# Performance work log

Measured on AMD Instinct MI355X. Metric: run time of the kernel, lower is better.

## Reference

```python
import jax, jax.numpy as jnp
import numpy as np

N = 16000      # nodes
E = 256000     # edges (avg degree 16)
C = 64         # channel multiplicity (64x0e node feats)
A = 10         # num elements (one-hot node_attrs)
R = 8          # num radial edge feats
OFFS = [0, 1, 4, 9]   # m-offsets for l=0,1,2 blocks (dims 1,3,5)
AVG_NEIGH = 16.0


def setup_inputs() -> dict:
    key = jax.random.key(0)
    ks = jax.random.split(key, 12)
    species = jax.random.randint(ks[0], (N,), 0, A)
    node_attrs = jax.nn.one_hot(species, A, dtype=jnp.float32)
    node_feats = jax.random.normal(ks[1], (N, C), jnp.float32)
    edge_attrs_real = jax.random.normal(ks[2], (E, 9), jnp.float32)
    edge_attrs_imag = jax.random.normal(ks[3], (E, 9), jnp.float32)
    edge_feats = jax.random.normal(ks[4], (E, R), jnp.float32)
    senders = jax.random.randint(ks[5], (E,), 0, N)
    receivers = jax.random.randint(ks[6], (E,), 0, N)
    # learned parameters
    W_up = jax.random.normal(ks[7], (C, C), jnp.float32)            # linear_up (64x0e -> 64x0e)
    W_tpw = jax.random.normal(ks[8], (A, R, 3, C), jnp.float32) * 0.1  # TensorProductWeightsBlock, weight_numel = 3*C
    W_lin = jax.random.normal(ks[9], (3, C, C), jnp.float32)        # per-l linear on irreps_mid -> irreps_out
    W_skip = jax.random.normal(ks[10], (C, A, C), jnp.float32)      # FullyConnectedTensorProduct skip
    return {"node_attrs": node_attrs, "node_feats": node_feats,
            "edge_attrs_real": edge_attrs_real, "edge_attrs_imag": edge_attrs_imag,
            "edge_feats": edge_feats, "senders": senders, "receivers": receivers,
            "W_up": W_up, "W_tpw": W_tpw, "W_lin": W_lin, "W_skip": W_skip}


def reference(node_attrs, node_feats, edge_attrs_real, edge_attrs_imag, edge_feats,
              senders, receivers, W_up, W_tpw, W_lin, W_skip):
    # skip connection: FullyConnectedTensorProduct(node_feats, node_attrs) (all scalars)
    sc = jnp.einsum('nu,na,uak->nk', node_feats, node_attrs, W_skip) / np.float32(np.sqrt(C * A))
    # linear_up (e3nn Linear with 1/sqrt(fan_in) normalization)
    h = (node_feats @ W_up) / np.float32(np.sqrt(C))
    # per-edge TP weights: einsum('be,ba,aek->bk'), reshaped to [E, 3 paths, C]
    tp_w = jnp.einsum('er,ea,arlu->elu', edge_feats, node_attrs[senders], W_tpw)
    x_s = h[senders]  # gather sender node feats [E, C]
    def conv(edge_attrs):
        # uvu tensor product 64x0e x (0e+1o+2e): CG(0,l,l)=1 -> weighted outer product per l
        parts = [x_s[:, :, None] * tp_w[:, l, :, None] * edge_attrs[:, None, OFFS[l]:OFFS[l + 1]]
                 for l in range(3)]
        mji = jnp.concatenate(parts, axis=-1)                      # [E, C, 9]
        m = jax.ops.segment_sum(mji, receivers, num_segments=N)   # scatter-sum -> [N, C, 9]
        outs = [jnp.einsum('num,uv->nvm', m[:, :, OFFS[l]:OFFS[l + 1]], W_lin[l]) / np.float32(np.sqrt(C))
                for l in range(3)]
        return jnp.concatenate(outs, axis=-1) / np.float32(AVG_NEIGH)  # [N, C, 9]
    message_real = conv(edge_attrs_real)
    message_imag = conv(edge_attrs_imag)
    # torch.view_as_complex + reshape_irreps -> complex [N, C, 9]; returned as (real, imag)
    return message_real, message_imag, sc
```

## Files before the change

### kernel.cpp

```cpp
#include <hip/hip_runtime.h>
#include <hip/hip_bf16.h>

#define NN 16000
#define EE 256000
#define CC 64
#define AA 10
#define RR 8
#define NC9 9216000
#define SC_OFF 18432000

#define WS_H        0
#define WS_BLK      4096000
#define WS_WLT      32768000
#define WS_SPECIES  32817152
#define WS_COUNTS   32881152
#define WS_CURSOR   32945152
#define WS_OFFSETS  33009152
#define WS_ELIST    33073216

__device__ __forceinline__ float comp4(float4 v, int j) {
  return j == 0 ? v.x : j == 1 ? v.y : j == 2 ? v.z : v.w;
}

__global__ __launch_bounds__(256) void prep_kernel(
    const float* __restrict__ attrs, const int* __restrict__ recv,
    const float* __restrict__ W_lin, int* __restrict__ species,
    int* __restrict__ counts, float* __restrict__ wlt) {
  int i = blockIdx.x * 256 + threadIdx.x;
  if (i < NN) {
    const float* p = attrs + (size_t)i * AA;
    int sp = 0;
#pragma unroll
    for (int a = 1; a < AA; ++a)
      if (p[a] > 0.5f) sp = a;
    species[i] = sp;
  }
  if (i < 3 * 64 * 64) {
    int l = i >> 12, rem = i & 4095, v = rem >> 6, u = rem & 63;
    wlt[i] = W_lin[l * 4096 + u * 64 + v];
  }
  if (i < EE) atomicAdd(&counts[recv[i]], 1);
}

__global__ __launch_bounds__(1024) void scan_kernel(
    const int* __restrict__ counts, int* __restrict__ offsets) {
  __shared__ int part[1024];
  int tid = threadIdx.x;
  const int CH = 16;
  int base = tid * CH;
  int loc[CH];
  int s = 0;
#pragma unroll
  for (int i = 0; i < CH; ++i) {
    int idx = base + i;
    int c = (idx < NN) ? counts[idx] : 0;
    loc[i] = c;
    s += c;
  }
  part[tid] = s;
  __syncthreads();
  for (int off = 1; off < 1024; off <<= 1) {
    int t = part[tid];
    int add = (tid >= off) ? part[tid - off] : 0;
    __syncthreads();
    part[tid] = t + add;
    __syncthreads();
  }
  int pre = (tid > 0) ? part[tid - 1] : 0;
#pragma unroll
  for (int i = 0; i < CH; ++i) {
    int idx = base + i;
    if (idx <= NN) offsets[idx] = pre;
    pre += loc[i];
  }
}

__global__ __launch_bounds__(256) void edge_kernel(
    const int* __restrict__ recv, const int* __restrict__ senders,
    const int* __restrict__ species, const int* __restrict__ offsets,
    int* __restrict__ cursor, int* __restrict__ elist,
    const float* __restrict__ ef, const float* __restrict__ ear,
    const float* __restrict__ eai, float* __restrict__ blk) {
  int e = blockIdx.x * 256 + threadIdx.x;
  if (e >= EE) return;
  int r = recv[e];
  int pos = atomicAdd(&cursor[r], 1);
  elist[offsets[r] + pos] = e;
  int s = senders[e];
  int a = species[s];
  const float* efp = ef + (size_t)e * 8;
  const float* erp = ear + (size_t)e * 9;
  const float* eip = eai + (size_t)e * 9;
  float4* dst = (float4*)(blk + (size_t)e * 28);
  float4 q;
  q.x = __int_as_float(s | (a << 20)); q.y = efp[0]; q.z = efp[1]; q.w = efp[2];
  dst[0] = q;
  q.x = efp[3]; q.y = efp[4]; q.z = efp[5]; q.w = efp[6];
  dst[1] = q;
  q.x = efp[7]; q.y = erp[0]; q.z = erp[1]; q.w = erp[2];
  dst[2] = q;
  q.x = erp[3]; q.y = erp[4]; q.z = erp[5]; q.w = erp[6];
  dst[3] = q;
  q.x = erp[7]; q.y = erp[8]; q.z = eip[0]; q.w = eip[1];
  dst[4] = q;
  q.x = eip[2]; q.y = eip[3]; q.z = eip[4]; q.w = eip[5];
  dst[5] = q;
  q.x = eip[6]; q.y = eip[7]; q.z = eip[8]; q.w = 0.f;
  dst[6] = q;
}

__global__ __launch_bounds__(256) void node_kernel(
    const float* __restrict__ nf, const float* __restrict__ attrs,
    const float* __restrict__ W_up, const float* __restrict__ W_skip,
    float* __restrict__ h, float* __restrict__ out) {
  __shared__ float sW[4096];
  for (int t = threadIdx.x; t < 4096; t += 256) sW[t] = W_up[t];
  __syncthreads();
  int wid = __builtin_amdgcn_readfirstlane(threadIdx.x >> 6);
  int lane = threadIdx.x & 63;
  for (int n = blockIdx.x * 4 + wid; n < NN; n += 4000) {
    const float* ap = attrs + (size_t)n * AA;
    int a = 0;
#pragma unroll
    for (int j = 1; j < AA; ++j)
      if (ap[j] > 0.5f) a = j;
    const float* nfp = nf + (size_t)n * 64;
    const float* wsk = W_skip + (size_t)a * 64;
    float hacc = 0.f, sacc = 0.f;
#pragma unroll
    for (int u = 0; u < 64; ++u) {
      float x = nfp[u];
      hacc = fmaf(x, sW[u * 64 + lane], hacc);
      sacc = fmaf(x, wsk[u * 640 + lane], sacc);
    }
    h[(size_t)n * 64 + lane] = hacc * 0.125f;
    out[SC_OFF + (size_t)n * 64 + lane] = sacc * 0.03952847075210474f;
  }
}

#define RLF(V, L) __int_as_float(__builtin_amdgcn_readlane((V), (L)))

#define EDGE2(EFA, ERA, EIA, PKV, XS) do {                                 \
  int a_ = (PKV) >> 20;                                                    \
  const float4* wp_ = (const float4*)(lds + a_ * 1792 + lane * 28);        \
  float4 w_[6];                                                            \
  _Pragma("unroll") for (int g_ = 0; g_ < 6; ++g_) w_[g_] = wp_[gpi[g_]];  \
  float t0_ = 0.f, t1_ = 0.f, t2_ = 0.f;                                   \
  _Pragma("unroll") for (int r_ = 0; r_ < 8; ++r_) {                       \
    t0_ = fmaf((EFA)[r_], comp4(w_[(r_ * 3 + 0) >> 2], (r_ * 3 + 0) & 3), t0_); \
    t1_ = fmaf((EFA)[r_], comp4(w_[(r_ * 3 + 1) >> 2], (r_ * 3 + 1) & 3), t1_); \
    t2_ = fmaf((EFA)[r_], comp4(w_[(r_ * 3 + 2) >> 2], (r_ * 3 + 2) & 3), t2_); \
  }                                                                        \
  t0_ *= (XS); t1_ *= (XS); t2_ *= (XS);                                   \
  accR[0] = fmaf(t0_, (ERA)[0], accR[0]);                                  \
  accI[0] = fmaf(t0_, (EIA)[0], accI[0]);                                  \
  _Pragma("unroll") for (int m_ = 1; m_ < 4; ++m_) {                       \
    accR[m_] = fmaf(t1_, (ERA)[m_], accR[m_]);                             \
    accI[m_] = fmaf(t1_, (EIA)[m_], accI[m_]);                             \
  }                                                                        \
  _Pragma("unroll") for (int m_ = 4; m_ < 9; ++m_) {                       \
    accR[m_] = fmaf(t2_, (ERA)[m_], accR[m_]);                             \
    accI[m_] = fmaf(t2_, (EIA)[m_], accI[m_]);                             \
  }                                                                        \
} while (0)

#define MIXL(LV, M0, M1)                                                    \
  _Pragma("unroll") for (int q_ = 0; q_ < 16; ++q_) {                       \
    float4 w4_ = *(const float4*)&lds[(LV) * 4096 + lane * 64 +             \
                                      ((q_ + lane) & 15) * 4];              \
    _Pragma("unroll") for (int j_ = 0; j_ < 4; ++j_) {                      \
      float wu_ = comp4(w4_, j_);                                           \
      _Pragma("unroll") for (int m_ = (M0); m_ < (M1); ++m_) {              \
        outR[m_] = fmaf(RLF(__float_as_int(accR[m_]), q_ * 4 + j_), wu_, outR[m_]); \
        outI[m_] = fmaf(RLF(__float_as_int(accI[m_]), q_ * 4 + j_), wu_, outI[m_]); \
      }                                                                     \
    }                                                                       \
  }

__global__ __launch_bounds__(512, 4) void fused_kernel(
    const float* __restrict__ h, const int* __restrict__ offs,
    const float* __restrict__ blkd, const int* __restrict__ elist,
    const float* __restrict__ W_tpw, const float* __restrict__ wlt,
    float* __restrict__ out) {
  __shared__ float lds[17920];
  for (int t = threadIdx.x; t < AA * 6 * 64; t += 512) {
    int a = t / 384, rem = t - a * 384;
    int g = rem >> 6, u = rem & 63;
    int gp = (g + 5 * u) % 7;
    const float* src = W_tpw + a * 1536 + g * 256 + u;
    float4 w;
    w.x = src[0]; w.y = src[64]; w.z = src[128]; w.w = src[192];
    *(float4*)&lds[a * 1792 + u * 28 + gp * 4] = w;
  }
  __syncthreads();
  int wid = __builtin_amdgcn_readfirstlane(threadIdx.x >> 6);
  int lane = threadIdx.x & 63;
  int n = blockIdx.x * 8 + wid;
  int gpi[6];
#pragma unroll
  for (int g = 0; g < 6; ++g) gpi[g] = (g + 5 * lane) % 7;
  float accR[9], accI[9];
#pragma unroll
  for (int m = 0; m < 9; ++m) { accR[m] = 0.f; accI[m] = 0.f; }
  int beg = __builtin_amdgcn_readfirstlane(offs[n]);
  int end_ = __builtin_amdgcn_readfirstlane(offs[n + 1]);
  if (end_ > beg) {
    const int* bi = (const int*)blkd;
    int e0 = elist[beg];
    int pk0 = bi[(size_t)e0 * 28];
    int e1 = (beg + 1 < end_) ? elist[beg + 1] : e0;
    int pk1 = bi[(size_t)e1 * 28];
    float xs0 = h[(size_t)(pk0 & 0xFFFFF) * 64 + lane];
    float xs1 = h[(size_t)(pk1 & 0xFFFFF) * 64 + lane];
    float efc[8], erc[9], eic[9];
    {
      const float* ep = blkd + (size_t)e0 * 28;
#pragma unroll
      for (int i = 0; i < 8; ++i) efc[i] = ep[1 + i];
#pragma unroll
      for (int i = 0; i < 9; ++i) erc[i] = ep[9 + i];
#pragma unroll
      for (int i = 0; i < 9; ++i) eic[i] = ep[18 + i];
    }
    for (int idx = beg; idx < end_; ++idx) {
      int e2 = e0, pk2 = pk0;
      float xs2 = 0.f;
      if (idx + 2 < end_) {
        e2 = elist[idx + 2];
        pk2 = bi[(size_t)e2 * 28];
        xs2 = h[(size_t)(pk2 & 0xFFFFF) * 64 + lane];
      }
      float efn[8], ern[9], ein[9];
      if (idx + 1 < end_) {
        const float* ep = blkd + (size_t)e1 * 28;
#pragma unroll
        for (int i = 0; i < 8; ++i) efn[i] = ep[1 + i];
#pragma unroll
        for (int i = 0; i < 9; ++i) ern[i] = ep[9 + i];
#pragma unroll
        for (int i = 0; i < 9; ++i) ein[i] = ep[18 + i];
      } else {
#pragma unroll
        for (int i = 0; i < 8; ++i) efn[i] = 0.f;
#pragma unroll
        for (int i = 0; i < 9; ++i) { ern[i] = 0.f; ein[i] = 0.f; }
      }
      EDGE2(efc, erc, eic, pk0, xs0);
      pk0 = pk1; xs0 = xs1;
      e1 = e2; pk1 = pk2; xs1 = xs2;
#pragma unroll
      for (int i = 0; i < 8; ++i) efc[i] = efn[i];
#pragma unroll
      for (int i = 0; i < 9; ++i) { erc[i] = ern[i]; eic[i] = ein[i]; }
    }
  }
  __builtin_amdgcn_sched_barrier(0);
  __syncthreads();
  for (int t = threadIdx.x; t < 3072; t += 512) {
    int l = t >> 10, rem = t & 1023, v = rem >> 4, q = rem & 15;
    int slot = (q + v) & 15;
    float4 w = *(const float4*)(wlt + l * 4096 + v * 64 + q * 4);
    *(float4*)&lds[l * 4096 + v * 64 + slot * 4] = w;
  }
  __syncthreads();
  float outR[9], outI[9];
#pragma unroll
  for (int m = 0; m < 9; ++m) { outR[m] = 0.f; outI[m] = 0.f; }
  MIXL(0, 0, 1)
  MIXL(1, 1, 4)
  MIXL(2, 4, 9)
  const float SCL = 0.0078125f;
  float* stg = lds + 12288 + wid * 576;
#pragma unroll
  for (int m = 0; m < 9; ++m) stg[lane * 9 + m] = outR[m] * SCL;
  __builtin_amdgcn_s_waitcnt(0);
#pragma unroll
  for (int k = 0; k < 9; ++k)
    out[(size_t)n * 576 + k * 64 + lane] = stg[k * 64 + lane];
#pragma unroll
  for (int m = 0; m < 9; ++m) stg[lane * 9 + m] = outI[m] * SCL;
  __builtin_amdgcn_s_waitcnt(0);
#pragma unroll
  for (int k = 0; k < 9; ++k)
    out[NC9 + (size_t)n * 576 + k * 64 + lane] = stg[k * 64 + lane];
}

extern "C" void kernel_launch(void* const* d_in, const int* in_sizes, int n_in,
                              void* d_out, int out_size, void* d_ws, size_t ws_size,
                              hipStream_t stream) {
  const float* node_attrs = (const float*)d_in[0];
  const float* node_feats = (const float*)d_in[1];
  const float* ear        = (const float*)d_in[2];
  const float* eai        = (const float*)d_in[3];
  const float* ef         = (const float*)d_in[4];
  const int*   senders    = (const int*)d_in[5];
  const int*   receivers  = (const int*)d_in[6];
  const float* W_up       = (const float*)d_in[7];
  const float* W_tpw      = (const float*)d_in[8];
  const float* W_lin      = (const float*)d_in[9];
  const float* W_skip     = (const float*)d_in[10];
  float* out = (float*)d_out;

  char* ws = (char*)d_ws;
  float* h        = (float*)(ws + WS_H);
  float* blk      = (float*)(ws + WS_BLK);
  float* wlt      = (float*)(ws + WS_WLT);
  int*   species  = (int*)(ws + WS_SPECIES);
  int*   counts   = (int*)(ws + WS_COUNTS);
  int*   cursor   = (int*)(ws + WS_CURSOR);
  int*   offsets  = (int*)(ws + WS_OFFSETS);
  int*   elist    = (int*)(ws + WS_ELIST);

  hipMemsetAsync(ws + WS_COUNTS, 0, 128000, stream);

  prep_kernel<<<1000, 256, 0, stream>>>(node_attrs, receivers, W_lin,
                                        species, counts, wlt);
  scan_kernel<<<1, 1024, 0, stream>>>(counts, offsets);
  edge_kernel<<<1000, 256, 0, stream>>>(receivers, senders, species, offsets,
                                        cursor, elist, ef, ear, eai, blk);
  node_kernel<<<1000, 256, 0, stream>>>(node_feats, node_attrs, W_up, W_skip,
                                        h, out);
  fused_kernel<<<2000, 512, 0, stream>>>(h, offsets, blk, elist, W_tpw, wlt,
                                         out);
}
```

Baseline: 348.4 us.

## Store edge blocks in receiver-sorted order, degree-sort nodes, fold node kernel into prep

The edge kernel now writes each packed edge record directly at its CSR slot, so the fused kernel streams contiguous edge data instead of indirecting through an edge list. The scan kernel builds a degree histogram and the edge kernel fills a permutation that orders nodes by descending degree. Each wave then processes nodes in that order, which balances work across waves. The separate node kernel (linear_up and skip) is merged into prep_kernel to save one launch. The cost is extra atomics for the permutation, and prep blocks now also load W_up into shared memory.

After: 351.6 us. Within noise of the previous version (+0.9%).

```diff
diff --git a/kernel.cpp b/kernel.cpp
--- a/kernel.cpp
+++ b/kernel.cpp
@@ -11,12 +11,14 @@
 
 #define WS_H        0
 #define WS_BLK      4096000
-#define WS_WLT      32768000
-#define WS_SPECIES  32817152
-#define WS_COUNTS   32881152
-#define WS_CURSOR   32945152
-#define WS_OFFSETS  33009152
-#define WS_ELIST    33073216
+#define WS_WLT      32768256
+#define WS_SPECIES  32817408
+#define WS_COUNTS   32881408
+#define WS_CURSOR   32945408
+#define WS_OFFSETS  33009408
+#define WS_PERM     33073472
+#define WS_DSTART   33137472
+#define WS_DEGCUR   33137728
 
 __device__ __forceinline__ float comp4(float4 v, int j) {
   return j == 0 ? v.x : j == 1 ? v.y : j == 2 ? v.z : v.w;
@@ -24,8 +26,13 @@
 
 __global__ __launch_bounds__(256) void prep_kernel(
     const float* __restrict__ attrs, const int* __restrict__ recv,
-    const float* __restrict__ W_lin, int* __restrict__ species,
-    int* __restrict__ counts, float* __restrict__ wlt) {
+    const float* __restrict__ W_lin, const float* __restrict__ nf,
+    const float* __restrict__ W_up, const float* __restrict__ W_skip,
+    int* __restrict__ species, int* __restrict__ counts,
+    float* __restrict__ wlt, float* __restrict__ h, float* __restrict__ out) {
+  __shared__ float sW[4096];
+  for (int t = threadIdx.x; t < 4096; t += 256) sW[t] = W_up[t];
+  __syncthreads();
   int i = blockIdx.x * 256 + threadIdx.x;
   if (i < NN) {
     const float* p = attrs + (size_t)i * AA;
@@ -40,12 +47,35 @@
     wlt[i] = W_lin[l * 4096 + u * 64 + v];
   }
   if (i < EE) atomicAdd(&counts[recv[i]], 1);
+  int wid = __builtin_amdgcn_readfirstlane(threadIdx.x >> 6);
+  int lane = threadIdx.x & 63;
+  for (int n = blockIdx.x * 4 + wid; n < NN; n += 4000) {
+    const float* ap = attrs + (size_t)n * AA;
+    int a = 0;
+#pragma unroll
+    for (int j = 1; j < AA; ++j)
+      if (ap[j] > 0.5f) a = j;
+    const float* nfp = nf + (size_t)n * 64;
+    const float* wsk = W_skip + (size_t)a * 64;
+    float hacc = 0.f, sacc = 0.f;
+#pragma unroll
+    for (int u = 0; u < 64; ++u) {
+      float x = nfp[u];
+      hacc = fmaf(x, sW[u * 64 + lane], hacc);
+      sacc = fmaf(x, wsk[u * 640 + lane], sacc);
+    }
+    h[(size_t)n * 64 + lane] = hacc * 0.125f;
+    out[SC_OFF + (size_t)n * 64 + lane] = sacc * 0.03952847075210474f;
+  }
 }
 
 __global__ __launch_bounds__(1024) void scan_kernel(
-    const int* __restrict__ counts, int* __restrict__ offsets) {
+    const int* __restrict__ counts, int* __restrict__ offsets,
+    int* __restrict__ dstart, int* __restrict__ degcur) {
   __shared__ int part[1024];
+  __shared__ int hist[64];
   int tid = threadIdx.x;
+  if (tid < 64) { hist[tid] = 0; degcur[tid] = 0; }
   const int CH = 16;
   int base = tid * CH;
   int loc[CH];
@@ -72,26 +102,39 @@
     int idx = base + i;
     if (idx <= NN) offsets[idx] = pre;
     pre += loc[i];
+    if (idx < NN) atomicAdd(&hist[min(loc[i], 63)], 1);
+  }
+  __syncthreads();
+  if (tid == 0) {
+    int run = 0;
+    for (int d = 63; d >= 0; --d) { dstart[d] = run; run += hist[d]; }
   }
 }
 
 __global__ __launch_bounds__(256) void edge_kernel(
     const int* __restrict__ recv, const int* __restrict__ senders,
     const int* __restrict__ species, const int* __restrict__ offsets,
-    int* __restrict__ cursor, int* __restrict__ elist,
-    const float* __restrict__ ef, const float* __restrict__ ear,
-    const float* __restrict__ eai, float* __restrict__ blk) {
+    int* __restrict__ cursor, const int* __restrict__ counts,
+    const int* __restrict__ dstart, int* __restrict__ degcur,
+    int* __restrict__ perm, const float* __restrict__ ef,
+    const float* __restrict__ ear, const float* __restrict__ eai,
+    float* __restrict__ blk) {
   int e = blockIdx.x * 256 + threadIdx.x;
+  if (e < NN) {
+    int d = min(counts[e], 63);
+    int pos = atomicAdd(&degcur[d], 1);
+    perm[dstart[d] + pos] = e;
+  }
   if (e >= EE) return;
   int r = recv[e];
   int pos = atomicAdd(&cursor[r], 1);
-  elist[offsets[r] + pos] = e;
+  int slot = offsets[r] + pos;
   int s = senders[e];
   int a = species[s];
   const float* efp = ef + (size_t)e * 8;
   const float* erp = ear + (size_t)e * 9;
   const float* eip = eai + (size_t)e * 9;
-  float4* dst = (float4*)(blk + (size_t)e * 28);
+  float4* dst = (float4*)(blk + (size_t)slot * 28);
   float4 q;
   q.x = __int_as_float(s | (a << 20)); q.y = efp[0]; q.z = efp[1]; q.w = efp[2];
   dst[0] = q;
@@ -107,35 +150,6 @@
   dst[5] = q;
   q.x = eip[6]; q.y = eip[7]; q.z = eip[8]; q.w = 0.f;
   dst[6] = q;
-}
-
-__global__ __launch_bounds__(256) void node_kernel(
-    const float* __restrict__ nf, const float* __restrict__ attrs,
-    const float* __restrict__ W_up, const float* __restrict__ W_skip,
-    float* __restrict__ h, float* __restrict__ out) {
-  __shared__ float sW[4096];
-  for (int t = threadIdx.x; t < 4096; t += 256) sW[t] = W_up[t];
-  __syncthreads();
-  int wid = __builtin_amdgcn_readfirstlane(threadIdx.x >> 6);
-  int lane = threadIdx.x & 63;
-  for (int n = blockIdx.x * 4 + wid; n < NN; n += 4000) {
-    const float* ap = attrs + (size_t)n * AA;
-    int a = 0;
-#pragma unroll
-    for (int j = 1; j < AA; ++j)
-      if (ap[j] > 0.5f) a = j;
-    const float* nfp = nf + (size_t)n * 64;
-    const float* wsk = W_skip + (size_t)a * 64;
-    float hacc = 0.f, sacc = 0.f;
-#pragma unroll
-    for (int u = 0; u < 64; ++u) {
-      float x = nfp[u];
-      hacc = fmaf(x, sW[u * 64 + lane], hacc);
-      sacc = fmaf(x, wsk[u * 640 + lane], sacc);
-    }
-    h[(size_t)n * 64 + lane] = hacc * 0.125f;
-    out[SC_OFF + (size_t)n * 64 + lane] = sacc * 0.03952847075210474f;
-  }
 }
 
 #define RLF(V, L) __int_as_float(__builtin_amdgcn_readlane((V), (L)))
@@ -179,7 +193,7 @@
 
 __global__ __launch_bounds__(512, 4) void fused_kernel(
     const float* __restrict__ h, const int* __restrict__ offs,
-    const float* __restrict__ blkd, const int* __restrict__ elist,
+    const float* __restrict__ blkd, const int* __restrict__ perm,
     const float* __restrict__ W_tpw, const float* __restrict__ wlt,
     float* __restrict__ out) {
   __shared__ float lds[17920];
@@ -195,7 +209,7 @@
   __syncthreads();
   int wid = __builtin_amdgcn_readfirstlane(threadIdx.x >> 6);
   int lane = threadIdx.x & 63;
-  int n = blockIdx.x * 8 + wid;
+  int n = __builtin_amdgcn_readfirstlane(perm[blockIdx.x * 8 + wid]);
   int gpi[6];
 #pragma unroll
   for (int g = 0; g < 6; ++g) gpi[g] = (g + 5 * lane) % 7;
@@ -206,15 +220,13 @@
   int end_ = __builtin_amdgcn_readfirstlane(offs[n + 1]);
   if (end_ > beg) {
     const int* bi = (const int*)blkd;
-    int e0 = elist[beg];
-    int pk0 = bi[(size_t)e0 * 28];
-    int e1 = (beg + 1 < end_) ? elist[beg + 1] : e0;
-    int pk1 = bi[(size_t)e1 * 28];
+    int pk0 = bi[(size_t)beg * 28];
+    int pk1 = (beg + 1 < end_) ? bi[(size_t)(beg + 1) * 28] : pk0;
     float xs0 = h[(size_t)(pk0 & 0xFFFFF) * 64 + lane];
     float xs1 = h[(size_t)(pk1 & 0xFFFFF) * 64 + lane];
     float efc[8], erc[9], eic[9];
     {
-      const float* ep = blkd + (size_t)e0 * 28;
+      const float* ep = blkd + (size_t)beg * 28;
 #pragma unroll
       for (int i = 0; i < 8; ++i) efc[i] = ep[1 + i];
 #pragma unroll
@@ -223,16 +235,15 @@
       for (int i = 0; i < 9; ++i) eic[i] = ep[18 + i];
     }
     for (int idx = beg; idx < end_; ++idx) {
-      int e2 = e0, pk2 = pk0;
+      int pk2 = pk0;
       float xs2 = 0.f;
       if (idx + 2 < end_) {
-        e2 = elist[idx + 2];
-        pk2 = bi[(size_t)e2 * 28];
+        pk2 = bi[(size_t)(idx + 2) * 28];
         xs2 = h[(size_t)(pk2 & 0xFFFFF) * 64 + lane];
       }
       float efn[8], ern[9], ein[9];
       if (idx + 1 < end_) {
-        const float* ep = blkd + (size_t)e1 * 28;
+        const float* ep = blkd + (size_t)(idx + 1) * 28;
 #pragma unroll
         for (int i = 0; i < 8; ++i) efn[i] = ep[1 + i];
 #pragma unroll
@@ -247,7 +258,7 @@
       }
       EDGE2(efc, erc, eic, pk0, xs0);
       pk0 = pk1; xs0 = xs1;
-      e1 = e2; pk1 = pk2; xs1 = xs2;
+      pk1 = pk2; xs1 = xs2;
 #pragma unroll
       for (int i = 0; i < 8; ++i) efc[i] = efn[i];
 #pragma unroll
@@ -309,17 +320,19 @@
   int*   counts   = (int*)(ws + WS_COUNTS);
   int*   cursor   = (int*)(ws + WS_CURSOR);
   int*   offsets  = (int*)(ws + WS_OFFSETS);
-  int*   elist    = (int*)(ws + WS_ELIST);
+  int*   perm     = (int*)(ws + WS_PERM);
+  int*   dstart   = (int*)(ws + WS_DSTART);
+  int*   degcur   = (int*)(ws + WS_DEGCUR);
 
   hipMemsetAsync(ws + WS_COUNTS, 0, 128000, stream);
 
   prep_kernel<<<1000, 256, 0, stream>>>(node_attrs, receivers, W_lin,
-                                        species, counts, wlt);
-  scan_kernel<<<1, 1024, 0, stream>>>(counts, offsets);
+                                        node_feats, W_up, W_skip,
+                                        species, counts, wlt, h, out);
+  scan_kernel<<<1, 1024, 0, stream>>>(counts, offsets, dstart, degcur);
   edge_kernel<<<1000, 256, 0, stream>>>(receivers, senders, species, offsets,
-                                        cursor, elist, ef, ear, eai, blk);
-  node_kernel<<<1000, 256, 0, stream>>>(node_feats, node_attrs, W_up, W_skip,
-                                        h, out);
-  fused_kernel<<<2000, 512, 0, stream>>>(h, offsets, blk, elist, W_tpw, wlt,
+                                        cursor, counts, dstart, degcur, perm,
+                                        ef, ear, eai, blk);
+  fused_kernel<<<2000, 512, 0, stream>>>(h, offsets, blk, perm, W_tpw, wlt,
                                          out);
 }
```
